# Optimization experiments

Hardware: AMD Instinct MI355X
Metric: run time of the kernel (lower is better)

Reference implementation:

```python
import jax, jax.numpy as jnp
import numpy as np

B, T, E, A = 4, 4096, 256, 64

def setup_inputs() -> dict:
    key = jax.random.key(0)
    ks = jax.random.split(key, 7)
    s = 1.0 / np.sqrt(E)
    return {
        "embedded": jax.random.normal(ks[0], (B, T, E), dtype=jnp.float32),
        "Wk": jax.random.normal(ks[1], (E, A), dtype=jnp.float32) * s,
        "bk": jax.random.normal(ks[2], (A,), dtype=jnp.float32) * s,
        "Wq": jax.random.normal(ks[3], (E, A), dtype=jnp.float32) * s,
        "bq": jax.random.normal(ks[4], (A,), dtype=jnp.float32) * s,
        "Wv": jax.random.normal(ks[5], (E, A), dtype=jnp.float32) * s,
        "bv": jax.random.normal(ks[6], (A,), dtype=jnp.float32) * s,
    }

def reference(embedded, Wk, bk, Wq, bq, Wv, bv):
    k = embedded @ Wk + bk                      # [B,T,A]
    q = embedded @ Wq + bq
    v = embedded @ Wv + bv
    scale = 1.0 / jnp.sqrt(jnp.asarray(k.shape[-1], dtype=k.dtype))
    scores = jnp.einsum('bqa,bka->bqk', q, k) * scale   # [B,T,T]
    Tn = scores.shape[-1]
    causal = jnp.tril(jnp.ones((Tn, Tn), dtype=bool))
    scores = jnp.where(causal, scores, -jnp.inf)
    sm = jax.nn.softmax(scores, axis=-1)
    return jnp.einsum('bqk,bka->bqa', sm, v)            # [B,T,A]
```

## Files before the change

### kernel.cpp

```cpp
#include <hip/hip_runtime.h>
#include <math.h>

#define Bn 4
#define Tn 4096
#define En 256
#define An 64
#define PLS 72
#define WLS 264

typedef __attribute__((ext_vector_type(8))) short short8;
typedef __attribute__((ext_vector_type(8))) __bf16 bf16x8;
typedef __attribute__((ext_vector_type(4))) float f32x4;
typedef __attribute__((ext_vector_type(4))) short short4v;
typedef __attribute__((ext_vector_type(2))) unsigned int uint2v;

__device__ __forceinline__ f32x4 mfma16(short8 a, short8 b, f32x4 c) {
    return __builtin_amdgcn_mfma_f32_16x16x32_bf16(
        __builtin_bit_cast(bf16x8, a), __builtin_bit_cast(bf16x8, b), c, 0, 0, 0);
}
__device__ __forceinline__ unsigned short f2bf(float x) {
    return __builtin_bit_cast(unsigned short, (__bf16)x);
}
__device__ __forceinline__ float bf2f(unsigned short h) {
    return __builtin_bit_cast(float, (unsigned int)h << 16);
}
__device__ __forceinline__ unsigned int packbf2(float lo, float hi) {
    return (unsigned int)f2bf(lo) | ((unsigned int)f2bf(hi) << 16);
}

__global__ __launch_bounds__(256, 2) void proj_kernel(
    const float* __restrict__ emb,
    const float* __restrict__ Wq, const float* __restrict__ Wk, const float* __restrict__ Wv,
    const float* __restrict__ bq, const float* __restrict__ bk, const float* __restrict__ bv,
    unsigned short* __restrict__ qg, unsigned short* __restrict__ kg,
    unsigned short* __restrict__ v_t)
{
    const int bid  = blockIdx.x;
    const int tid  = threadIdx.x;
    const int wave = tid >> 6, lane = tid & 63, quad = lane >> 4, l15 = lane & 15;
    const int jh   = bid & 1;
    const int rb   = bid >> 1;
    const int row0  = rb * 64;
    const int b     = row0 >> 12;
    const int trow0 = row0 & 4095;

    __shared__ unsigned short Wl[96 * WLS];
    __shared__ unsigned short vtr[64 * PLS];

    {
        const float* __restrict__ srcA = jh ? Wv : Wq;
        const int lrbA = jh ? 32 : 0;
#pragma unroll
        for (int it = 0; it < 16; it++) {
            const int idx = it * 256 + tid;
            const int col = idx & 63;
            const int e0  = (idx >> 6) * 4;
            const float w0 = srcA[(size_t)(e0 + 0) * An + col];
            const float w1 = srcA[(size_t)(e0 + 1) * An + col];
            const float w2 = srcA[(size_t)(e0 + 2) * An + col];
            const float w3 = srcA[(size_t)(e0 + 3) * An + col];
            *(short4v*)&Wl[(lrbA + col) * WLS + e0] =
                (short4v){(short)f2bf(w0), (short)f2bf(w1), (short)f2bf(w2), (short)f2bf(w3)};
        }
        const int coloff = jh ? 32 : 0;
        const int lrbB   = jh ? 0 : 64;
#pragma unroll
        for (int it = 0; it < 8; it++) {
            const int idx = it * 256 + tid;
            const int col = idx & 31;
            const int e0  = (idx >> 5) * 4;
            const float w0 = Wk[(size_t)(e0 + 0) * An + coloff + col];
            const float w1 = Wk[(size_t)(e0 + 1) * An + coloff + col];
            const float w2 = Wk[(size_t)(e0 + 2) * An + coloff + col];
            const float w3 = Wk[(size_t)(e0 + 3) * An + coloff + col];
            *(short4v*)&Wl[(lrbB + col) * WLS + e0] =
                (short4v){(short)f2bf(w0), (short)f2bf(w1), (short)f2bf(w2), (short)f2bf(w3)};
        }
    }

    short8 A[8];
    {
        const float* erow = emb + (size_t)(row0 + wave * 16 + l15) * En;
#pragma unroll
        for (int c = 0; c < 8; c++) {
            const float* pp = erow + c * 32 + quad * 8;
            float4 f0 = *(const float4*)pp;
            float4 f1 = *(const float4*)(pp + 4);
            A[c] = (short8){(short)f2bf(f0.x), (short)f2bf(f0.y), (short)f2bf(f0.z), (short)f2bf(f0.w),
                            (short)f2bf(f1.x), (short)f2bf(f1.y), (short)f2bf(f1.z), (short)f2bf(f1.w)};
        }
    }
    __syncthreads();

    f32x4 acc[6];
#pragma unroll
    for (int x = 0; x < 6; x++) acc[x] = (f32x4){0.f, 0.f, 0.f, 0.f};

#pragma unroll
    for (int x = 0; x < 6; x++) {
        const unsigned short* wrow = &Wl[(x * 16 + l15) * WLS];
#pragma unroll
        for (int c = 0; c < 8; c++)
            acc[x] = mfma16(A[c], *(const short8*)(wrow + c * 32 + quad * 8), acc[x]);
    }

    const float QS = 0.125f * 1.4426950408889634f;
#pragma unroll
    for (int x = 0; x < 6; x++) {
        const int nt = jh * 6 + x;
        const int m  = nt >> 2;
        const int al = (nt & 3) * 16 + l15;
        const float bsv = ((m == 0) ? bq : (m == 1) ? bk : bv)[al];
#pragma unroll
        for (int rg = 0; rg < 4; rg++) {
            const int row_l = wave * 16 + quad * 4 + rg;
            const float val = acc[x][rg] + bsv;
            if (m == 0)      qg[(size_t)(row0 + row_l) * An + al] = f2bf(val * QS);
            else if (m == 1) kg[(size_t)(row0 + row_l) * An + al] = f2bf(val);
            else             vtr[al * PLS + row_l] = f2bf(val);
        }
    }
    if (jh == 1) {
        __syncthreads();
        const int a  = tid >> 2;
        const int tg = (tid & 3) * 16;
        unsigned short* dst = v_t + (size_t)(b * 64 + a) * Tn + trow0 + tg;
        *(short8*)dst       = *(const short8*)&vtr[a * PLS + tg];
        *(short8*)(dst + 8) = *(const short8*)&vtr[a * PLS + tg + 8];
    }
}

__global__ __launch_bounds__(256, 2) void flash_kernel(
    const unsigned short* __restrict__ qg, const unsigned short* __restrict__ kg,
    const unsigned short* __restrict__ v_t,
    unsigned short* __restrict__ Opart, float* __restrict__ Lp,
    int S, int lgS)
{
    const int b    = blockIdx.y;
    const int tid  = threadIdx.x;
    const int wave = tid >> 6, lane = tid & 63, quad = lane >> 4, l15 = lane & 15;
    const int ub   = blockIdx.x;
    const int S4   = S >> 2;
    const int p    = ub >> (lgS - 2);
    const int sb   = ub & (S4 - 1);
    const int s    = sb * 4 + wave;

    __shared__ unsigned short lds[4 * 64 * PLS];
    __shared__ float lW[4][64];
    unsigned short* tw = lds + wave * (64 * PLS);

    const unsigned short* kb0 = kg  + ((size_t)b << 12) * An;
    const unsigned short* vb0 = v_t + (size_t)b * An * Tn;

#pragma unroll 1
    for (int tile = 0; tile < 2; tile++) {
        const int qt    = tile ? (63 - p) : p;
        const int qrow0 = qt * 64;
        const int tmax  = qt;

        short8 qB[4][2];
        {
            const unsigned short* qb = qg + (((size_t)b << 12) + qrow0) * An;
#pragma unroll
            for (int g = 0; g < 4; g++)
#pragma unroll
                for (int c = 0; c < 2; c++)
                    qB[g][c] = *(const short8*)(qb + (size_t)(16 * g + l15) * An + c * 32 + quad * 8);
        }

        float lacc[4] = {0.f, 0.f, 0.f, 0.f};
        f32x4 O[4][4];
#pragma unroll
        for (int nt = 0; nt < 4; nt++)
#pragma unroll
            for (int g = 0; g < 4; g++) O[nt][g] = (f32x4){0.f, 0.f, 0.f, 0.f};

        int t = s;
        if (t <= tmax) {
            short8 KA[4][2];
            {
                const unsigned short* kb = kb0 + (size_t)t * (64 * An);
#pragma unroll
                for (int nt = 0; nt < 4; nt++)
#pragma unroll
                    for (int c = 0; c < 2; c++)
                        KA[nt][c] = *(const short8*)(kb + (nt * 16 + l15) * An + c * 32 + quad * 8);
            }
            for (;;) {
                short8 VA[4][2];
                {
                    const unsigned short* vb = vb0 + (size_t)t * 64;
#pragma unroll
                    for (int nt = 0; nt < 4; nt++)
#pragma unroll
                        for (int c = 0; c < 2; c++)
                            VA[nt][c] = *(const short8*)(vb + (size_t)(nt * 16 + l15) * Tn + c * 32 + quad * 8);
                }

                const int tn = t + S;
                const bool more = (tn <= tmax);
                short8 KN[4][2];
                if (more) {
                    const unsigned short* kb = kb0 + (size_t)tn * (64 * An);
#pragma unroll
                    for (int nt = 0; nt < 4; nt++)
#pragma unroll
                        for (int c = 0; c < 2; c++)
                            KN[nt][c] = *(const short8*)(kb + (nt * 16 + l15) * An + c * 32 + quad * 8);
                }

                const bool diag = (t == tmax);

#pragma unroll
                for (int g = 0; g < 4; g++) {
                    f32x4 St[4];
#pragma unroll
                    for (int nt = 0; nt < 4; nt++) {
                        f32x4 a0 = (f32x4){0.f, 0.f, 0.f, 0.f};
                        a0 = mfma16(KA[nt][0], qB[g][0], a0);
                        a0 = mfma16(KA[nt][1], qB[g][1], a0);
                        St[nt] = a0;
                    }
                    if (diag) {
                        const int qr = 16 * g + l15;
                        const int kvb = quad * 4;
#pragma unroll
                        for (int nt = 0; nt < 4; nt++)
#pragma unroll
                            for (int rg = 0; rg < 4; rg++)
                                if (nt * 16 + kvb + rg > qr) St[nt][rg] = -__builtin_inff();
                    }
                    float rs = 0.f;
#pragma unroll
                    for (int nt = 0; nt < 4; nt++) {
                        const float p0 = exp2f(St[nt][0]);
                        const float p1 = exp2f(St[nt][1]);
                        const float p2 = exp2f(St[nt][2]);
                        const float p3 = exp2f(St[nt][3]);
                        rs += (p0 + p1) + (p2 + p3);
                        const unsigned int d0 = packbf2(p0, p1);
                        const unsigned int d1 = packbf2(p2, p3);
                        *(short4v*)&tw[(16 * g + l15) * PLS + 16 * nt + quad * 4] =
                            __builtin_bit_cast(short4v, (uint2v){d0, d1});
                    }
                    lacc[g] += rs;
#pragma unroll
                    for (int c = 0; c < 2; c++) {
                        const short8 pb = *(const short8*)&tw[(16 * g + l15) * PLS + c * 32 + quad * 8];
#pragma unroll
                        for (int nt = 0; nt < 4; nt++)
                            O[nt][g] = mfma16(VA[nt][c], pb, O[nt][g]);
                    }
                }

                if (!more) break;
                t = tn;
#pragma unroll
                for (int nt = 0; nt < 4; nt++)
#pragma unroll
                    for (int c = 0; c < 2; c++) KA[nt][c] = KN[nt][c];
            }
        }

#pragma unroll
        for (int nt = 0; nt < 4; nt++)
#pragma unroll
            for (int g = 0; g < 4; g++) {
                const unsigned int d0 = packbf2(O[nt][g][0], O[nt][g][1]);
                const unsigned int d1 = packbf2(O[nt][g][2], O[nt][g][3]);
                *(short4v*)&tw[(16 * g + l15) * PLS + 16 * nt + quad * 4] =
                    __builtin_bit_cast(short4v, (uint2v){d0, d1});
            }
#pragma unroll
        for (int g = 0; g < 4; g++) {
            lacc[g] += __shfl_xor(lacc[g], 16);
            lacc[g] += __shfl_xor(lacc[g], 32);
        }
        if (quad == 0) {
#pragma unroll
            for (int g = 0; g < 4; g++) lW[wave][16 * g + l15] = lacc[g];
        }
        __syncthreads();

        {
            const int row = tid >> 2;
            const int a16 = (tid & 3) * 16;
            float acc[16];
#pragma unroll
            for (int x = 0; x < 16; x++) acc[x] = 0.f;
            float lsum = 0.f;
#pragma unroll
            for (int w = 0; w < 4; w++) {
                const unsigned short* src = lds + w * (64 * PLS) + row * PLS + a16;
                const short8 o0 = *(const short8*)src;
                const short8 o1 = *(const short8*)(src + 8);
#pragma unroll
                for (int x = 0; x < 8; x++) {
                    acc[x]     += bf2f((unsigned short)o0[x]);
                    acc[8 + x] += bf2f((unsigned short)o1[x]);
                }
                lsum += lW[w][row];
            }
            const size_t unit = (size_t)(b * 64 + qt) * (size_t)S4 + sb;
            unsigned short* ob = Opart + unit * 4096 + row * 64 + a16;
            short8 r0, r1;
#pragma unroll
            for (int x = 0; x < 8; x++) {
                r0[x] = (short)f2bf(acc[x]);
                r1[x] = (short)f2bf(acc[8 + x]);
            }
            *(short8*)ob       = r0;
            *(short8*)(ob + 8) = r1;
            if ((tid & 3) == 0) Lp[unit * 64 + row] = lsum;
        }
        __syncthreads();
    }
}

__global__ __launch_bounds__(256) void merge_kernel(
    const unsigned short* __restrict__ Opart, const float* __restrict__ Lp,
    float* __restrict__ out, int S4)
{
    const int qt = blockIdx.x, b = blockIdx.y;
    const int tid = threadIdx.x;
    const int qr  = tid >> 2;
    const int a16 = (tid & 3) * 16;
    const size_t ub = (size_t)(b * 64 + qt) * (size_t)S4;

    float acc[16];
#pragma unroll
    for (int x = 0; x < 16; x++) acc[x] = 0.f;
    float lsum = 0.f;

#pragma unroll 1
    for (int sb = 0; sb < S4; sb++) {
        const unsigned short* op = &Opart[(ub + sb) * 4096 + qr * 64 + a16];
        const short8 o0 = *(const short8*)op;
        const short8 o1 = *(const short8*)(op + 8);
#pragma unroll
        for (int x = 0; x < 8; x++) {
            acc[x]     += bf2f((unsigned short)o0[x]);
            acc[8 + x] += bf2f((unsigned short)o1[x]);
        }
        lsum += Lp[(ub + sb) * 64 + qr];
    }
    const float inv = 1.f / lsum;
    float* o = out + (((size_t)b << 12) + qt * 64 + qr) * An + a16;
#pragma unroll
    for (int h = 0; h < 4; h++) {
        float4 r = {acc[h * 4] * inv, acc[h * 4 + 1] * inv,
                    acc[h * 4 + 2] * inv, acc[h * 4 + 3] * inv};
        *(float4*)(o + h * 4) = r;
    }
}

extern "C" void kernel_launch(void* const* d_in, const int* in_sizes, int n_in,
                              void* d_out, int out_size, void* d_ws, size_t ws_size,
                              hipStream_t stream) {
    const float* emb = (const float*)d_in[0];
    const float* Wk  = (const float*)d_in[1];
    const float* bk  = (const float*)d_in[2];
    const float* Wq  = (const float*)d_in[3];
    const float* bq  = (const float*)d_in[4];
    const float* Wv  = (const float*)d_in[5];
    const float* bv  = (const float*)d_in[6];
    float* out = (float*)d_out;

    char* ws = (char*)d_ws;
    const size_t MB = 1024 * 1024;

    int S = 8, lgS = 3;
    if (7 * MB + (size_t)256 * 8 * 4096 * 2 <= ws_size)      { S = 32; lgS = 5; }
    else if (7 * MB + (size_t)256 * 4 * 4096 * 2 <= ws_size) { S = 16; lgS = 4; }
    const int S4 = S >> 2;

    unsigned short* q     = (unsigned short*)(ws);
    unsigned short* k     = (unsigned short*)(ws + 2 * MB);
    unsigned short* v_t   = (unsigned short*)(ws + 4 * MB);
    float*          Lp    = (float*)(ws + 6 * MB);
    unsigned short* Opart = (unsigned short*)(ws + 7 * MB);

    proj_kernel<<<512, 256, 0, stream>>>(emb, Wq, Wk, Wv, bq, bk, bv, q, k, v_t);
    flash_kernel<<<dim3(8 * S, 4), 256, 0, stream>>>(q, k, v_t, Opart, Lp, S, lgS);
    merge_kernel<<<dim3(64, 4), 256, 0, stream>>>(Opart, Lp, out, S4);
}
```

Before: 143.6 us.

## Pre-transpose weights in separate kernel, add MFMA priority hints, widen merge grid

Adds a small kernel that converts and transposes Wq/Wk/Wv to bf16 once, folding the query scale into the weights. The projection kernel then reads weights straight from global memory instead of staging them in LDS per block. The flash kernel wraps its MFMA groups in s_setprio hints, and the merge kernel moves to a grid four times larger with one float4 per thread. The split count is capped at 16 instead of 32. This adds one more launch, and the direct global weight reads may hit cache less well than LDS.

```diff
diff --git a/kernel.cpp b/kernel.cpp
--- a/kernel.cpp
+++ b/kernel.cpp
@@ -6,7 +6,6 @@
 #define En 256
 #define An 64
 #define PLS 72
-#define WLS 264
 
 typedef __attribute__((ext_vector_type(8))) short short8;
 typedef __attribute__((ext_vector_type(8))) __bf16 bf16x8;
@@ -14,6 +13,8 @@
 typedef __attribute__((ext_vector_type(4))) short short4v;
 typedef __attribute__((ext_vector_type(2))) unsigned int uint2v;
 
+#define QSCALE (0.125f * 1.4426950408889634f)
+
 __device__ __forceinline__ f32x4 mfma16(short8 a, short8 b, f32x4 c) {
     return __builtin_amdgcn_mfma_f32_16x16x32_bf16(
         __builtin_bit_cast(bf16x8, a), __builtin_bit_cast(bf16x8, b), c, 0, 0, 0);
@@ -28,9 +29,32 @@
     return (unsigned int)f2bf(lo) | ((unsigned int)f2bf(hi) << 16);
 }
 
+__global__ __launch_bounds__(256) void wprep_kernel(
+    const float* __restrict__ Wq, const float* __restrict__ Wk,
+    const float* __restrict__ Wv, unsigned short* __restrict__ Wt)
+{
+    const int bx = blockIdx.x, tid = threadIdx.x;
+    const int m = bx >> 2, e0 = (bx & 3) * 64;
+    const float* __restrict__ W = (m == 0) ? Wq : (m == 1) ? Wk : Wv;
+    const float sc = (m == 0) ? QSCALE : 1.0f;
+
+    __shared__ unsigned short t[64][72];
+    const int a_in = tid & 63;
+#pragma unroll
+    for (int it = 0; it < 16; it++) {
+        const int el = it * 4 + (tid >> 6);
+        t[a_in][el] = f2bf(W[(size_t)(e0 + el) * An + a_in] * sc);
+    }
+    __syncthreads();
+    const int a  = tid >> 2;
+    const int eg = (tid & 3) * 16;
+    unsigned short* dst = Wt + ((size_t)(m * 64 + a) << 8) + e0 + eg;
+    *(short8*)dst       = *(const short8*)&t[a][eg];
+    *(short8*)(dst + 8) = *(const short8*)&t[a][eg + 8];
+}
+
 __global__ __launch_bounds__(256, 2) void proj_kernel(
-    const float* __restrict__ emb,
-    const float* __restrict__ Wq, const float* __restrict__ Wk, const float* __restrict__ Wv,
+    const float* __restrict__ emb, const unsigned short* __restrict__ Wt,
     const float* __restrict__ bq, const float* __restrict__ bk, const float* __restrict__ bv,
     unsigned short* __restrict__ qg, unsigned short* __restrict__ kg,
     unsigned short* __restrict__ v_t)
@@ -44,39 +68,7 @@
     const int b     = row0 >> 12;
     const int trow0 = row0 & 4095;
 
-    __shared__ unsigned short Wl[96 * WLS];
     __shared__ unsigned short vtr[64 * PLS];
-
-    {
-        const float* __restrict__ srcA = jh ? Wv : Wq;
-        const int lrbA = jh ? 32 : 0;
-#pragma unroll
-        for (int it = 0; it < 16; it++) {
-            const int idx = it * 256 + tid;
-            const int col = idx & 63;
-            const int e0  = (idx >> 6) * 4;
-            const float w0 = srcA[(size_t)(e0 + 0) * An + col];
-            const float w1 = srcA[(size_t)(e0 + 1) * An + col];
-            const float w2 = srcA[(size_t)(e0 + 2) * An + col];
-            const float w3 = srcA[(size_t)(e0 + 3) * An + col];
-            *(short4v*)&Wl[(lrbA + col) * WLS + e0] =
-                (short4v){(short)f2bf(w0), (short)f2bf(w1), (short)f2bf(w2), (short)f2bf(w3)};
-        }
-        const int coloff = jh ? 32 : 0;
-        const int lrbB   = jh ? 0 : 64;
-#pragma unroll
-        for (int it = 0; it < 8; it++) {
-            const int idx = it * 256 + tid;
-            const int col = idx & 31;
-            const int e0  = (idx >> 5) * 4;
-            const float w0 = Wk[(size_t)(e0 + 0) * An + coloff + col];
-            const float w1 = Wk[(size_t)(e0 + 1) * An + coloff + col];
-            const float w2 = Wk[(size_t)(e0 + 2) * An + coloff + col];
-            const float w3 = Wk[(size_t)(e0 + 3) * An + coloff + col];
-            *(short4v*)&Wl[(lrbB + col) * WLS + e0] =
-                (short4v){(short)f2bf(w0), (short)f2bf(w1), (short)f2bf(w2), (short)f2bf(w3)};
-        }
-    }
 
     short8 A[8];
     {
@@ -90,32 +82,33 @@
                             (short)f2bf(f1.x), (short)f2bf(f1.y), (short)f2bf(f1.z), (short)f2bf(f1.w)};
         }
     }
-    __syncthreads();
 
     f32x4 acc[6];
 #pragma unroll
     for (int x = 0; x < 6; x++) acc[x] = (f32x4){0.f, 0.f, 0.f, 0.f};
 
-#pragma unroll
-    for (int x = 0; x < 6; x++) {
-        const unsigned short* wrow = &Wl[(x * 16 + l15) * WLS];
-#pragma unroll
-        for (int c = 0; c < 8; c++)
-            acc[x] = mfma16(A[c], *(const short8*)(wrow + c * 32 + quad * 8), acc[x]);
-    }
-
-    const float QS = 0.125f * 1.4426950408889634f;
 #pragma unroll
     for (int x = 0; x < 6; x++) {
         const int nt = jh * 6 + x;
         const int m  = nt >> 2;
         const int al = (nt & 3) * 16 + l15;
-        const float bsv = ((m == 0) ? bq : (m == 1) ? bk : bv)[al];
+        const unsigned short* wrow = Wt + ((size_t)(m * 64 + al) << 8);
+#pragma unroll
+        for (int c = 0; c < 8; c++)
+            acc[x] = mfma16(A[c], *(const short8*)(wrow + c * 32 + quad * 8), acc[x]);
+    }
+
+#pragma unroll
+    for (int x = 0; x < 6; x++) {
+        const int nt = jh * 6 + x;
+        const int m  = nt >> 2;
+        const int al = (nt & 3) * 16 + l15;
+        const float bsv = (m == 0) ? bq[al] * QSCALE : ((m == 1) ? bk : bv)[al];
 #pragma unroll
         for (int rg = 0; rg < 4; rg++) {
             const int row_l = wave * 16 + quad * 4 + rg;
             const float val = acc[x][rg] + bsv;
-            if (m == 0)      qg[(size_t)(row0 + row_l) * An + al] = f2bf(val * QS);
+            if (m == 0)      qg[(size_t)(row0 + row_l) * An + al] = f2bf(val);
             else if (m == 1) kg[(size_t)(row0 + row_l) * An + al] = f2bf(val);
             else             vtr[al * PLS + row_l] = f2bf(val);
         }
@@ -214,6 +207,7 @@
 #pragma unroll
                 for (int g = 0; g < 4; g++) {
                     f32x4 St[4];
+                    __builtin_amdgcn_s_setprio(1);
 #pragma unroll
                     for (int nt = 0; nt < 4; nt++) {
                         f32x4 a0 = (f32x4){0.f, 0.f, 0.f, 0.f};
@@ -221,6 +215,7 @@
                         a0 = mfma16(KA[nt][1], qB[g][1], a0);
                         St[nt] = a0;
                     }
+                    __builtin_amdgcn_s_setprio(0);
                     if (diag) {
                         const int qr = 16 * g + l15;
                         const int kvb = quad * 4;
@@ -247,9 +242,11 @@
 #pragma unroll
                     for (int c = 0; c < 2; c++) {
                         const short8 pb = *(const short8*)&tw[(16 * g + l15) * PLS + c * 32 + quad * 8];
+                        __builtin_amdgcn_s_setprio(1);
 #pragma unroll
                         for (int nt = 0; nt < 4; nt++)
                             O[nt][g] = mfma16(VA[nt][c], pb, O[nt][g]);
+                        __builtin_amdgcn_s_setprio(0);
                     }
                 }
 
@@ -321,37 +318,27 @@
     const unsigned short* __restrict__ Opart, const float* __restrict__ Lp,
     float* __restrict__ out, int S4)
 {
-    const int qt = blockIdx.x, b = blockIdx.y;
+    const int bx = blockIdx.x, b = blockIdx.y;
+    const int qt = bx >> 2, qq = bx & 3;
     const int tid = threadIdx.x;
-    const int qr  = tid >> 2;
-    const int a16 = (tid & 3) * 16;
+    const int row = qq * 16 + (tid >> 4);
+    const int a4  = (tid & 15) * 4;
     const size_t ub = (size_t)(b * 64 + qt) * (size_t)S4;
 
-    float acc[16];
-#pragma unroll
-    for (int x = 0; x < 16; x++) acc[x] = 0.f;
+    float acc[4] = {0.f, 0.f, 0.f, 0.f};
     float lsum = 0.f;
-
-#pragma unroll 1
-    for (int sb = 0; sb < S4; sb++) {
-        const unsigned short* op = &Opart[(ub + sb) * 4096 + qr * 64 + a16];
-        const short8 o0 = *(const short8*)op;
-        const short8 o1 = *(const short8*)(op + 8);
-#pragma unroll
-        for (int x = 0; x < 8; x++) {
-            acc[x]     += bf2f((unsigned short)o0[x]);
-            acc[8 + x] += bf2f((unsigned short)o1[x]);
-        }
-        lsum += Lp[(ub + sb) * 64 + qr];
+    for (int sbi = 0; sbi < S4; sbi++) {
+        const short4v o = *(const short4v*)&Opart[(ub + sbi) * 4096 + row * 64 + a4];
+        acc[0] += bf2f((unsigned short)o[0]);
+        acc[1] += bf2f((unsigned short)o[1]);
+        acc[2] += bf2f((unsigned short)o[2]);
+        acc[3] += bf2f((unsigned short)o[3]);
+        lsum += Lp[(ub + sbi) * 64 + row];
     }
     const float inv = 1.f / lsum;
-    float* o = out + (((size_t)b << 12) + qt * 64 + qr) * An + a16;
-#pragma unroll
-    for (int h = 0; h < 4; h++) {
-        float4 r = {acc[h * 4] * inv, acc[h * 4 + 1] * inv,
-                    acc[h * 4 + 2] * inv, acc[h * 4 + 3] * inv};
-        *(float4*)(o + h * 4) = r;
-    }
+    float* o = out + (((size_t)b << 12) + qt * 64 + row) * An + a4;
+    float4 r = {acc[0] * inv, acc[1] * inv, acc[2] * inv, acc[3] * inv};
+    *(float4*)o = r;
 }
 
 extern "C" void kernel_launch(void* const* d_in, const int* in_sizes, int n_in,
@@ -370,17 +357,18 @@
     const size_t MB = 1024 * 1024;
 
     int S = 8, lgS = 3;
-    if (7 * MB + (size_t)256 * 8 * 4096 * 2 <= ws_size)      { S = 32; lgS = 5; }
-    else if (7 * MB + (size_t)256 * 4 * 4096 * 2 <= ws_size) { S = 16; lgS = 4; }
+    if (7 * MB + (size_t)1024 * 8192 <= ws_size) { S = 16; lgS = 4; }
     const int S4 = S >> 2;
 
     unsigned short* q     = (unsigned short*)(ws);
     unsigned short* k     = (unsigned short*)(ws + 2 * MB);
     unsigned short* v_t   = (unsigned short*)(ws + 4 * MB);
-    float*          Lp    = (float*)(ws + 6 * MB);
+    unsigned short* Wt    = (unsigned short*)(ws + 6 * MB);
+    float*          Lp    = (float*)(ws + 6 * MB + 128 * 1024);
     unsigned short* Opart = (unsigned short*)(ws + 7 * MB);
 
-    proj_kernel<<<512, 256, 0, stream>>>(emb, Wq, Wk, Wv, bq, bk, bv, q, k, v_t);
+    wprep_kernel<<<12, 256, 0, stream>>>(Wq, Wk, Wv, Wt);
+    proj_kernel<<<512, 256, 0, stream>>>(emb, Wt, bq, bk, bv, q, k, v_t);
     flash_kernel<<<dim3(8 * S, 4), 256, 0, stream>>>(q, k, v_t, Opart, Lp, S, lgS);
-    merge_kernel<<<dim3(64, 4), 256, 0, stream>>>(Opart, Lp, out, S4);
-}
+    merge_kernel<<<dim3(256, 4), 256, 0, stream>>>(Opart, Lp, out, S4);
+}
```

Result: no change. 141.2 us (-1.7%).

## Stream V loads into PV MFMAs, add setprio, rebalance split and merge grid

Applied to the files above, without the earlier changes.

The flash kernel no longer preloads all V fragments into registers per tile. It loads each V fragment just before its MFMA, wraps the MFMA groups in s_setprio, and relaxes launch bounds to one block per SIMD pair. The KV split count S is capped at 16 instead of 32, and the merge kernel uses four times more blocks with fewer accumulators per thread. The intent is to cut register pressure and merge overhead, at the risk of exposing V load latency inside the inner loop and lowering split parallelism.

```diff
diff --git a/kernel.cpp b/kernel.cpp
--- a/kernel.cpp
+++ b/kernel.cpp
@@ -130,7 +130,7 @@
     }
 }
 
-__global__ __launch_bounds__(256, 2) void flash_kernel(
+__global__ __launch_bounds__(256, 1) void flash_kernel(
     const unsigned short* __restrict__ qg, const unsigned short* __restrict__ kg,
     const unsigned short* __restrict__ v_t,
     unsigned short* __restrict__ Opart, float* __restrict__ Lp,
@@ -187,15 +187,7 @@
                         KA[nt][c] = *(const short8*)(kb + (nt * 16 + l15) * An + c * 32 + quad * 8);
             }
             for (;;) {
-                short8 VA[4][2];
-                {
-                    const unsigned short* vb = vb0 + (size_t)t * 64;
-#pragma unroll
-                    for (int nt = 0; nt < 4; nt++)
-#pragma unroll
-                        for (int c = 0; c < 2; c++)
-                            VA[nt][c] = *(const short8*)(vb + (size_t)(nt * 16 + l15) * Tn + c * 32 + quad * 8);
-                }
+                const unsigned short* vb = vb0 + (size_t)t * 64;
 
                 const int tn = t + S;
                 const bool more = (tn <= tmax);
@@ -214,6 +206,7 @@
 #pragma unroll
                 for (int g = 0; g < 4; g++) {
                     f32x4 St[4];
+                    __builtin_amdgcn_s_setprio(1);
 #pragma unroll
                     for (int nt = 0; nt < 4; nt++) {
                         f32x4 a0 = (f32x4){0.f, 0.f, 0.f, 0.f};
@@ -221,6 +214,7 @@
                         a0 = mfma16(KA[nt][1], qB[g][1], a0);
                         St[nt] = a0;
                     }
+                    __builtin_amdgcn_s_setprio(0);
                     if (diag) {
                         const int qr = 16 * g + l15;
                         const int kvb = quad * 4;
@@ -247,9 +241,13 @@
 #pragma unroll
                     for (int c = 0; c < 2; c++) {
                         const short8 pb = *(const short8*)&tw[(16 * g + l15) * PLS + c * 32 + quad * 8];
-#pragma unroll
-                        for (int nt = 0; nt < 4; nt++)
-                            O[nt][g] = mfma16(VA[nt][c], pb, O[nt][g]);
+                        __builtin_amdgcn_s_setprio(1);
+#pragma unroll
+                        for (int nt = 0; nt < 4; nt++) {
+                            const short8 va = *(const short8*)(vb + (size_t)(nt * 16 + l15) * Tn + c * 32 + quad * 8);
+                            O[nt][g] = mfma16(va, pb, O[nt][g]);
+                        }
+                        __builtin_amdgcn_s_setprio(0);
                     }
                 }
 
@@ -321,37 +319,27 @@
     const unsigned short* __restrict__ Opart, const float* __restrict__ Lp,
     float* __restrict__ out, int S4)
 {
-    const int qt = blockIdx.x, b = blockIdx.y;
+    const int bx = blockIdx.x, b = blockIdx.y;
+    const int qt = bx >> 2, qq = bx & 3;
     const int tid = threadIdx.x;
-    const int qr  = tid >> 2;
-    const int a16 = (tid & 3) * 16;
+    const int row = qq * 16 + (tid >> 4);
+    const int a4  = (tid & 15) * 4;
     const size_t ub = (size_t)(b * 64 + qt) * (size_t)S4;
 
-    float acc[16];
-#pragma unroll
-    for (int x = 0; x < 16; x++) acc[x] = 0.f;
+    float acc[4] = {0.f, 0.f, 0.f, 0.f};
     float lsum = 0.f;
-
-#pragma unroll 1
-    for (int sb = 0; sb < S4; sb++) {
-        const unsigned short* op = &Opart[(ub + sb) * 4096 + qr * 64 + a16];
-        const short8 o0 = *(const short8*)op;
-        const short8 o1 = *(const short8*)(op + 8);
-#pragma unroll
-        for (int x = 0; x < 8; x++) {
-            acc[x]     += bf2f((unsigned short)o0[x]);
-            acc[8 + x] += bf2f((unsigned short)o1[x]);
-        }
-        lsum += Lp[(ub + sb) * 64 + qr];
+    for (int sbi = 0; sbi < S4; sbi++) {
+        const short4v o = *(const short4v*)&Opart[(ub + sbi) * 4096 + row * 64 + a4];
+        acc[0] += bf2f((unsigned short)o[0]);
+        acc[1] += bf2f((unsigned short)o[1]);
+        acc[2] += bf2f((unsigned short)o[2]);
+        acc[3] += bf2f((unsigned short)o[3]);
+        lsum += Lp[(ub + sbi) * 64 + row];
     }
     const float inv = 1.f / lsum;
-    float* o = out + (((size_t)b << 12) + qt * 64 + qr) * An + a16;
-#pragma unroll
-    for (int h = 0; h < 4; h++) {
-        float4 r = {acc[h * 4] * inv, acc[h * 4 + 1] * inv,
-                    acc[h * 4 + 2] * inv, acc[h * 4 + 3] * inv};
-        *(float4*)(o + h * 4) = r;
-    }
+    float* o = out + (((size_t)b << 12) + qt * 64 + row) * An + a4;
+    float4 r = {acc[0] * inv, acc[1] * inv, acc[2] * inv, acc[3] * inv};
+    *(float4*)o = r;
 }
 
 extern "C" void kernel_launch(void* const* d_in, const int* in_sizes, int n_in,
@@ -370,8 +358,7 @@
     const size_t MB = 1024 * 1024;
 
     int S = 8, lgS = 3;
-    if (7 * MB + (size_t)256 * 8 * 4096 * 2 <= ws_size)      { S = 32; lgS = 5; }
-    else if (7 * MB + (size_t)256 * 4 * 4096 * 2 <= ws_size) { S = 16; lgS = 4; }
+    if (7 * MB + (size_t)1024 * 8192 <= ws_size) { S = 16; lgS = 4; }
     const int S4 = S >> 2;
 
     unsigned short* q     = (unsigned short*)(ws);
@@ -382,5 +369,5 @@
 
     proj_kernel<<<512, 256, 0, stream>>>(emb, Wq, Wk, Wv, bq, bk, bv, q, k, v_t);
     flash_kernel<<<dim3(8 * S, 4), 256, 0, stream>>>(q, k, v_t, Opart, Lp, S, lgS);
-    merge_kernel<<<dim3(64, 4), 256, 0, stream>>>(Opart, Lp, out, S4);
-}
+    merge_kernel<<<dim3(256, 4), 256, 0, stream>>>(Opart, Lp, out, S4);
+}
```

Measured after the change: 150.6 us. +4.8%, slower.
